# Kernel optimization log

Hardware: AMD Instinct MI355X
Metric: run time of the kernel (lower is better)

The kernel has to match this reference:

```python
import jax, jax.numpy as jnp
import numpy as np

H = 1024      # hidden_size
I = 2048      # intermediate_size
E = 32        # num_routed_experts
B, S = 4, 2048


def setup_inputs() -> dict:
    key = jax.random.key(0)
    ks = jax.random.split(key, 8)
    scale = 0.02
    inp = {
        "hidden_states": jax.random.normal(ks[0], (B, S, H), dtype=jnp.float32),
        # router gate: stored [H, E] so logits = x @ gate_w
        "gate_w": jax.random.normal(ks[1], (H, E), dtype=jnp.float32) * scale,
        # shared SwiGLU (num_shared_experts=1), weights stored [in, out]
        "shared_gate_w": jax.random.normal(ks[2], (H, I), dtype=jnp.float32) * scale,
        "shared_up_w": jax.random.normal(ks[3], (H, I), dtype=jnp.float32) * scale,
        "shared_down_w": jax.random.normal(ks[4], (I, H), dtype=jnp.float32) * scale,
        # routed grouped SwiGLU, weights stored [E, in, out] (matches GroupedLinear)
        "routed_gate_w": jax.random.normal(ks[5], (E, H, I), dtype=jnp.float32) * scale,
        "routed_up_w": jax.random.normal(ks[6], (E, H, I), dtype=jnp.float32) * scale,
        "routed_down_w": jax.random.normal(ks[7], (E, I, H), dtype=jnp.float32) * scale,
    }
    return inp


def _grouped_mm(a, w, group_sizes):
    # a: [T, in], w: [E, in, out], group_sizes: [E] int32 -> [T, out]
    return jax.lax.ragged_dot(a, w, group_sizes)


def _swiglu(x, gw, uw, dw):
    return (jax.nn.silu(x @ gw) * (x @ uw)) @ dw


def reference(hidden_states, gate_w, shared_gate_w, shared_up_w, shared_down_w,
              routed_gate_w, routed_up_w, routed_down_w):
    b, s, h = hidden_states.shape
    x = hidden_states.reshape(-1, h)                      # [T, H]

    # ---- shared expert ----
    shared_out = _swiglu(x, shared_gate_w, shared_up_w, shared_down_w)

    # ---- router: top-1 ----
    logits = x @ gate_w                                   # [T, E]
    topk_ids = jnp.argmax(logits, axis=-1)                # [T]
    topk_val = jnp.max(logits, axis=-1)                   # [T]
    scores = jax.nn.sigmoid(topk_val)[:, None]            # [T, 1]
    xs = x * scores                                       # scale tokens by router score

    # ---- dispatch: sort tokens by expert id ----
    tokens_per_expert = jnp.zeros((E,), jnp.int32).at[topk_ids].add(1)
    order = jnp.argsort(topk_ids)                         # token ids sorted by expert
    sorted_x = xs[order]                                  # [T, H]

    # ---- grouped SwiGLU experts ----
    g = _grouped_mm(sorted_x, routed_gate_w, tokens_per_expert)   # [T, I]
    u = _grouped_mm(sorted_x, routed_up_w, tokens_per_expert)     # [T, I]
    d = _grouped_mm(jax.nn.silu(g) * u, routed_down_w, tokens_per_expert)  # [T, H]

    # ---- combine: unsort back to token order ----
    inv = jnp.argsort(order)
    routed_out = d[inv]

    return (shared_out + routed_out).reshape(b, s, h)
```

## Files before the change

### kernel.cpp

```cpp
#include <hip/hip_runtime.h>
#include <stdint.h>
#include <stddef.h>

#define TOK 8192
#define H 1024
#define IDIM 2048
#define NE 32
#define BM 128
#define BN 64
#define BK 64
#define MAX_TILES 96

typedef __attribute__((ext_vector_type(8))) short short8;
typedef __attribute__((ext_vector_type(4))) float f32x4;
typedef __attribute__((ext_vector_type(4))) float float4v;
typedef __attribute__((ext_vector_type(2))) unsigned int uint2v;


__device__ __forceinline__ unsigned short f2bf(float x) {
  unsigned u = __builtin_bit_cast(unsigned, x);
  u += 0x7fffu + ((u >> 16) & 1u);
  return (unsigned short)(u >> 16);
}

__device__ __forceinline__ void gll16(const void* g, void* l) {
  __builtin_amdgcn_global_load_lds(
      (const __attribute__((address_space(1))) unsigned int*)g,
      (__attribute__((address_space(3))) unsigned int*)l, 16, 0, 0);
}

__device__ __forceinline__ f32x4 mfma16(short8 a, short8 b, f32x4 c) {
  return __builtin_amdgcn_mfma_f32_16x16x32_bf16(a, b, c, 0, 0, 0);
}

__device__ __forceinline__ int wswz(int n) {
  return ((n ^ (n >> 2)) & 7) << 4;
}


__global__ __launch_bounds__(256) void router_kernel(
    const float* __restrict__ x, const float* __restrict__ gw,
    unsigned short* __restrict__ xbf, unsigned short* __restrict__ xsbf,
    int* __restrict__ expert_id, int* __restrict__ counts)
{
  __shared__ float xl[8 * H];
  __shared__ float plog[8][8][NE];
  __shared__ float sscore[8];
  const int tid = threadIdx.x;
  const long t0 = (long)blockIdx.x * 8;

  const float4v* src = (const float4v*)(x + t0 * H);
  float4v* dst = (float4v*)xl;
  #pragma unroll
  for (int i = 0; i < 8; ++i) dst[tid + i * 256] = src[tid + i * 256];
  __syncthreads();

  {
    const int e = tid & 31, c = tid >> 5;
    float acc[8] = {0, 0, 0, 0, 0, 0, 0, 0};
    const float* gp = gw + (c * 128) * NE + e;
    for (int h = 0; h < 128; ++h) {
      float g = gp[h * NE];
      const float* xr = xl + (c * 128 + h);
      #pragma unroll
      for (int tk = 0; tk < 8; ++tk) acc[tk] += xr[tk * H] * g;
    }
    #pragma unroll
    for (int tk = 0; tk < 8; ++tk) plog[c][tk][e] = acc[tk];
  }
  __syncthreads();
  {
    const int e = tid & 31, tok = tid >> 5;
    float lg = 0.f;
    #pragma unroll
    for (int c = 0; c < 8; ++c) lg += plog[c][tok][e];
    float m = lg; int be = e;
    #pragma unroll
    for (int mask = 16; mask >= 1; mask >>= 1) {
      float om = __shfl_xor(m, mask);
      int   oe = __shfl_xor(be, mask);
      if (om > m || (om == m && oe < be)) { m = om; be = oe; }
    }
    if (e == 0) {
      sscore[tok] = 1.f / (1.f + __expf(-m));
      expert_id[t0 + tok] = be;
      atomicAdd(&counts[be], 1);
    }
  }
  __syncthreads();
  {
    const float sc = sscore[tid >> 5];
    const int base = (tid >> 5) * H + (tid & 31) * 32;
    #pragma unroll
    for (int i = 0; i < 4; ++i) {
      short8 vx, vs;
      #pragma unroll
      for (int j = 0; j < 8; ++j) {
        float v = xl[base + i * 8 + j];
        vx[j] = (short)f2bf(v);
        vs[j] = (short)f2bf(v * sc);
      }
      *(short8*)(xbf  + t0 * H + base + i * 8) = vx;
      *(short8*)(xsbf + t0 * H + base + i * 8) = vs;
    }
  }
}


__global__ void scan_kernel(const int* __restrict__ counts, int* __restrict__ offsets,
                            int* __restrict__ cursor, int* __restrict__ tile_e,
                            int* __restrict__ tile_p, int* __restrict__ n_tiles)
{
  if (threadIdx.x != 0) return;
  int off = 0, nt = 0;
  for (int e = 0; e < NE; ++e) {
    offsets[e] = off; cursor[e] = off;
    int cc = counts[e];
    for (int k = 0; k < cc; k += BM) { tile_e[nt] = e; tile_p[nt] = off + k; ++nt; }
    off += cc;
  }
  offsets[NE] = off;
  n_tiles[0] = nt;
}


__global__ __launch_bounds__(256) void perm_kernel(
    const int* __restrict__ expert_id, int* __restrict__ cursor, int* __restrict__ perm)
{
  int t = blockIdx.x * 256 + threadIdx.x;
  int e = expert_id[t];
  int pos = atomicAdd(&cursor[e], 1);
  perm[pos] = t;
}


template<bool ROUTED>
__global__ __launch_bounds__(256, 2) void gateup_kernel(
    const unsigned short* __restrict__ Abase,
    const float* __restrict__ WgAll, const float* __restrict__ WuAll,
    unsigned short* __restrict__ act,
    const int* __restrict__ perm, const int* __restrict__ tile_e,
    const int* __restrict__ tile_p, const int* __restrict__ offsets,
    const int* __restrict__ n_tiles)
{
  __shared__ short Alds[2][BM * BK];
  __shared__ short Glds[BN * BK];
  __shared__ short Ulds[BN * BK];

  const int tid = threadIdx.x;
  const int wave = tid >> 6, lane = tid & 63;

  int row0, row_end;
  const float *Wg, *Wu;
  if constexpr (ROUTED) {
    if ((int)blockIdx.x >= *n_tiles) return;
    const int e = tile_e[blockIdx.x];
    row0 = tile_p[blockIdx.x];
    row_end = offsets[e + 1];
    Wg = WgAll + (size_t)e * H * IDIM;
    Wu = WuAll + (size_t)e * H * IDIM;
  } else {
    row0 = blockIdx.x * BM; row_end = row0 + BM;
    Wg = WgAll; Wu = WuAll;
  }
  const int n0 = blockIdx.y * BN;

  const unsigned short* asrc[4];
  int aoff[4];
  #pragma unroll
  for (int i = 0; i < 4; ++i) {
    const int r = i * 32 + wave * 8 + (lane >> 3);
    int grow;
    if constexpr (ROUTED) {
      int p = row0 + r;
      if (p >= row_end) p = row0;
      grow = perm[p];
    } else grow = row0 + r;
    const int cb = ((lane & 7) * 16) ^ ((r & 7) << 4);
    asrc[i] = Abase + (size_t)grow * H + (cb >> 1);
    aoff[i] = (i * 32 + wave * 8) * BK;
  }

  const int wq = tid >> 4;
  const int wc = tid & 15;

  f32x4 accg[2][4] = {};
  f32x4 accu[2][4] = {};
  float4v g4[4], u4[4];

  auto stageA = [&](int k0, int buf) {
    #pragma unroll
    for (int i = 0; i < 4; ++i) gll16(asrc[i] + k0, &Alds[buf][aoff[i]]);
  };
  auto loadW = [&](int k0) {
    #pragma unroll
    for (int r = 0; r < 4; ++r) {
      const size_t goff = (size_t)(k0 + wq * 4 + r) * IDIM + (n0 + wc * 4);
      g4[r] = *(const float4v*)(Wg + goff);
      u4[r] = *(const float4v*)(Wu + goff);
    }
  };
  auto writeW = [&]() {
    #pragma unroll
    for (int j = 0; j < 4; ++j) {
      const int n = wc * 4 + j;
      const int cb = (wq * 8) ^ wswz(n);
      uint2v pg, pu;
      pg.x = (unsigned)f2bf(g4[0][j]) | ((unsigned)f2bf(g4[1][j]) << 16);
      pg.y = (unsigned)f2bf(g4[2][j]) | ((unsigned)f2bf(g4[3][j]) << 16);
      pu.x = (unsigned)f2bf(u4[0][j]) | ((unsigned)f2bf(u4[1][j]) << 16);
      pu.y = (unsigned)f2bf(u4[2][j]) | ((unsigned)f2bf(u4[3][j]) << 16);
      *(uint2v*)((char*)Glds + n * 128 + cb) = pg;
      *(uint2v*)((char*)Ulds + n * 128 + cb) = pu;
    }
  };
  auto compute = [&](int buf) {
    #pragma unroll
    for (int kk = 0; kk < 2; ++kk) {
      short8 af[2];
      #pragma unroll
      for (int m = 0; m < 2; ++m) {
        const int r = wave * 32 + m * 16 + (lane & 15);
        const int cb = (kk * 64 + ((lane >> 4) * 16)) ^ ((r & 7) << 4);
        af[m] = *(const short8*)((const char*)Alds[buf] + r * 128 + cb);
      }
      #pragma unroll
      for (int nf = 0; nf < 4; ++nf) {
        const int n = nf * 16 + (lane & 15);
        const int cb = (kk * 64 + ((lane >> 4) * 16)) ^ wswz(n);
        short8 bg = *(const short8*)((const char*)Glds + n * 128 + cb);
        short8 bu = *(const short8*)((const char*)Ulds + n * 128 + cb);
        #pragma unroll
        for (int m = 0; m < 2; ++m) {
          accg[m][nf] = mfma16(af[m], bg, accg[m][nf]);
          accu[m][nf] = mfma16(af[m], bu, accu[m][nf]);
        }
      }
    }
  };

  stageA(0, 0);
  loadW(0);
  writeW();
  __syncthreads();

  int cur = 0;
  #pragma unroll 1
  for (int kt = 0; kt < H / BK - 1; ++kt) {
    stageA((kt + 1) * BK, cur ^ 1);
    loadW((kt + 1) * BK);
    compute(cur);
    __syncthreads();
    writeW();
    __syncthreads();
    cur ^= 1;
  }
  compute(cur);

  #pragma unroll
  for (int m = 0; m < 2; ++m)
    #pragma unroll
    for (int nf = 0; nf < 4; ++nf) {
      const int col = n0 + nf * 16 + (lane & 15);
      #pragma unroll
      for (int j = 0; j < 4; ++j) {
        const int row = row0 + wave * 32 + m * 16 + ((lane >> 4) * 4) + j;
        if (ROUTED && row >= row_end) continue;
        const float g = accg[m][nf][j];
        const float u = accu[m][nf][j];
        const float v = (g / (1.f + __expf(-g))) * u;
        act[(size_t)row * IDIM + col] = f2bf(v);
      }
    }
}


template<bool ROUTED>
__global__ __launch_bounds__(256, 2) void down_kernel(
    const unsigned short* __restrict__ act,
    const float* __restrict__ WdAll,
    float* __restrict__ out,
    const int* __restrict__ perm, const int* __restrict__ tile_e,
    const int* __restrict__ tile_p, const int* __restrict__ offsets,
    const int* __restrict__ n_tiles)
{
  __shared__ short Alds[2][BM * BK];
  __shared__ short Wlds[BN * BK];

  const int tid = threadIdx.x;
  const int wave = tid >> 6, lane = tid & 63;

  int row0, row_end;
  const float* Wd;
  if constexpr (ROUTED) {
    if ((int)blockIdx.x >= *n_tiles) return;
    const int e = tile_e[blockIdx.x];
    row0 = tile_p[blockIdx.x];
    row_end = offsets[e + 1];
    Wd = WdAll + (size_t)e * IDIM * H;
  } else {
    row0 = blockIdx.x * BM; row_end = row0 + BM;
    Wd = WdAll;
  }
  const int n0 = blockIdx.y * BN;

  const unsigned short* asrc[4];
  int aoff[4];
  #pragma unroll
  for (int i = 0; i < 4; ++i) {
    const int r = i * 32 + wave * 8 + (lane >> 3);
    int p = row0 + r;
    if (ROUTED && p >= row_end) p = row0;
    const int cb = ((lane & 7) * 16) ^ ((r & 7) << 4);
    asrc[i] = act + (size_t)p * IDIM + (cb >> 1);
    aoff[i] = (i * 32 + wave * 8) * BK;
  }

  const int wq = tid >> 4;
  const int wc = tid & 15;

  f32x4 acc[2][4] = {};
  float4v w4[4];

  auto stageA = [&](int k0, int buf) {
    #pragma unroll
    for (int i = 0; i < 4; ++i) gll16(asrc[i] + k0, &Alds[buf][aoff[i]]);
  };
  auto loadW = [&](int k0) {
    #pragma unroll
    for (int r = 0; r < 4; ++r)
      w4[r] = *(const float4v*)(Wd + (size_t)(k0 + wq * 4 + r) * H + (n0 + wc * 4));
  };
  auto writeW = [&]() {
    #pragma unroll
    for (int j = 0; j < 4; ++j) {
      const int n = wc * 4 + j;
      const int cb = (wq * 8) ^ wswz(n);
      uint2v pw;
      pw.x = (unsigned)f2bf(w4[0][j]) | ((unsigned)f2bf(w4[1][j]) << 16);
      pw.y = (unsigned)f2bf(w4[2][j]) | ((unsigned)f2bf(w4[3][j]) << 16);
      *(uint2v*)((char*)Wlds + n * 128 + cb) = pw;
    }
  };
  auto compute = [&](int buf) {
    #pragma unroll
    for (int kk = 0; kk < 2; ++kk) {
      short8 af[2];
      #pragma unroll
      for (int m = 0; m < 2; ++m) {
        const int r = wave * 32 + m * 16 + (lane & 15);
        const int cb = (kk * 64 + ((lane >> 4) * 16)) ^ ((r & 7) << 4);
        af[m] = *(const short8*)((const char*)Alds[buf] + r * 128 + cb);
      }
      #pragma unroll
      for (int nf = 0; nf < 4; ++nf) {
        const int n = nf * 16 + (lane & 15);
        const int cb = (kk * 64 + ((lane >> 4) * 16)) ^ wswz(n);
        short8 bw = *(const short8*)((const char*)Wlds + n * 128 + cb);
        #pragma unroll
        for (int m = 0; m < 2; ++m) acc[m][nf] = mfma16(af[m], bw, acc[m][nf]);
      }
    }
  };

  stageA(0, 0);
  loadW(0);
  writeW();
  __syncthreads();

  int cur = 0;
  #pragma unroll 1
  for (int kt = 0; kt < IDIM / BK - 1; ++kt) {
    stageA((kt + 1) * BK, cur ^ 1);
    loadW((kt + 1) * BK);
    compute(cur);
    __syncthreads();
    writeW();
    __syncthreads();
    cur ^= 1;
  }
  compute(cur);

  #pragma unroll
  for (int m = 0; m < 2; ++m)
    #pragma unroll
    for (int nf = 0; nf < 4; ++nf) {
      const int col = n0 + nf * 16 + (lane & 15);
      #pragma unroll
      for (int j = 0; j < 4; ++j) {
        const int row = row0 + wave * 32 + m * 16 + ((lane >> 4) * 4) + j;
        const float v = acc[m][nf][j];
        if constexpr (ROUTED) {
          if (row < row_end) {
            const int t = perm[row];
            out[(size_t)t * H + col] += v;
          }
        } else {
          out[(size_t)row * H + col] = v;
        }
      }
    }
}


extern "C" void kernel_launch(void* const* d_in, const int* in_sizes, int n_in,
                              void* d_out, int out_size, void* d_ws, size_t ws_size,
                              hipStream_t stream) {
  (void)in_sizes; (void)n_in; (void)out_size; (void)ws_size;
  const float* x      = (const float*)d_in[0];
  const float* gate_w = (const float*)d_in[1];
  const float* sgw    = (const float*)d_in[2];
  const float* suw    = (const float*)d_in[3];
  const float* sdw    = (const float*)d_in[4];
  const float* rgw    = (const float*)d_in[5];
  const float* ruw    = (const float*)d_in[6];
  const float* rdw    = (const float*)d_in[7];
  float* out = (float*)d_out;

  char* ws = (char*)d_ws;
  unsigned short* xbf  = (unsigned short*)(ws + 0);
  unsigned short* xsbf = (unsigned short*)(ws + 16777216);
  unsigned short* act  = (unsigned short*)(ws + 33554432);
  int* perm      = (int*)(ws + 67108864);
  int* expert_id = (int*)(ws + 67141632);
  int* counts    = (int*)(ws + 67174400);
  int* offsets   = (int*)(ws + 67174528);
  int* cursor    = (int*)(ws + 67174784);
  int* tile_e    = (int*)(ws + 67174912);
  int* tile_p    = (int*)(ws + 67175424);
  int* n_tiles   = (int*)(ws + 67175936);

  hipMemsetAsync(counts, 0, NE * sizeof(int), stream);
  router_kernel<<<TOK / 8, 256, 0, stream>>>(x, gate_w, xbf, xsbf, expert_id, counts);
  scan_kernel<<<1, 64, 0, stream>>>(counts, offsets, cursor, tile_e, tile_p, n_tiles);
  perm_kernel<<<TOK / 256, 256, 0, stream>>>(expert_id, cursor, perm);

  gateup_kernel<false><<<dim3(TOK / BM, IDIM / BN), 256, 0, stream>>>(
      xbf, sgw, suw, act, perm, tile_e, tile_p, offsets, n_tiles);
  down_kernel<false><<<dim3(TOK / BM, H / BN), 256, 0, stream>>>(
      act, sdw, out, perm, tile_e, tile_p, offsets, n_tiles);
  gateup_kernel<true><<<dim3(MAX_TILES, IDIM / BN), 256, 0, stream>>>(
      xsbf, rgw, ruw, act, perm, tile_e, tile_p, offsets, n_tiles);
  down_kernel<true><<<dim3(MAX_TILES, H / BN), 256, 0, stream>>>(
      act, rdw, out, perm, tile_e, tile_p, offsets, n_tiles);
}
```

Baseline: 714.9 us.

## Widen GEMM N tile to 128 with a 2x2 wave layout per block

Doubles the output tile width from 64 to 128 columns and arranges the four waves in a 2x2 grid, each computing a 64x64 sub-tile (4x4 MFMA fragments). Each thread now loads 8 weight rows and writes 16-byte packed bf16 vectors into LDS. The aim is to reuse each staged A tile across twice as many columns, which halves the number of A reloads and blocks. In exchange, accumulator registers double (32 f32x4 for gate/up), which may push VGPR pressure against the launch bound of 2 blocks per CU, and the larger weight LDS tiles reduce occupancy headroom.

```diff
diff --git a/kernel.cpp b/kernel.cpp
--- a/kernel.cpp
+++ b/kernel.cpp
@@ -7,14 +7,14 @@
 #define IDIM 2048
 #define NE 32
 #define BM 128
-#define BN 64
+#define BN 128
 #define BK 64
 #define MAX_TILES 96
 
 typedef __attribute__((ext_vector_type(8))) short short8;
 typedef __attribute__((ext_vector_type(4))) float f32x4;
 typedef __attribute__((ext_vector_type(4))) float float4v;
-typedef __attribute__((ext_vector_type(2))) unsigned int uint2v;
+typedef __attribute__((ext_vector_type(4))) unsigned int uint4v;
 
 
 __device__ __forceinline__ unsigned short f2bf(float x) {
@@ -149,6 +149,7 @@
 
   const int tid = threadIdx.x;
   const int wave = tid >> 6, lane = tid & 63;
+  const int wm = wave >> 1, wn = wave & 1;
 
   int row0, row_end;
   const float *Wg, *Wu;
@@ -169,7 +170,7 @@
   int aoff[4];
   #pragma unroll
   for (int i = 0; i < 4; ++i) {
-    const int r = i * 32 + wave * 8 + (lane >> 3);
+    const int r = wave * 32 + i * 8 + (lane >> 3);
     int grow;
     if constexpr (ROUTED) {
       int p = row0 + r;
@@ -178,24 +179,26 @@
     } else grow = row0 + r;
     const int cb = ((lane & 7) * 16) ^ ((r & 7) << 4);
     asrc[i] = Abase + (size_t)grow * H + (cb >> 1);
-    aoff[i] = (i * 32 + wave * 8) * BK;
-  }
-
-  const int wq = tid >> 4;
-  const int wc = tid & 15;
-
-  f32x4 accg[2][4] = {};
-  f32x4 accu[2][4] = {};
-  float4v g4[4], u4[4];
-
-  auto stageA = [&](int k0, int buf) {
-    #pragma unroll
-    for (int i = 0; i < 4; ++i) gll16(asrc[i] + k0, &Alds[buf][aoff[i]]);
-  };
-  auto loadW = [&](int k0) {
-    #pragma unroll
-    for (int r = 0; r < 4; ++r) {
-      const size_t goff = (size_t)(k0 + wq * 4 + r) * IDIM + (n0 + wc * 4);
+    aoff[i] = (wave * 32 + i * 8) * BK;
+  }
+
+  const int wq = tid >> 5;
+  const int wc = tid & 31;
+
+  f32x4 accg[4][4] = {};
+  f32x4 accu[4][4] = {};
+  float4v g4[8], u4[8];
+
+  auto stageA = [&](int kt) {
+    short* base = Alds[kt & 1];
+    #pragma unroll
+    for (int i = 0; i < 4; ++i) gll16(asrc[i] + kt * BK, base + aoff[i]);
+  };
+  auto loadW = [&](int kt) {
+    const int k0 = kt * BK;
+    #pragma unroll
+    for (int r = 0; r < 8; ++r) {
+      const size_t goff = (size_t)(k0 + wq * 8 + r) * IDIM + (n0 + wc * 4);
       g4[r] = *(const float4v*)(Wg + goff);
       u4[r] = *(const float4v*)(Wu + goff);
     }
@@ -204,34 +207,39 @@
     #pragma unroll
     for (int j = 0; j < 4; ++j) {
       const int n = wc * 4 + j;
-      const int cb = (wq * 8) ^ wswz(n);
-      uint2v pg, pu;
+      const int cb = (wq * 16) ^ wswz(n);
+      uint4v pg, pu;
       pg.x = (unsigned)f2bf(g4[0][j]) | ((unsigned)f2bf(g4[1][j]) << 16);
       pg.y = (unsigned)f2bf(g4[2][j]) | ((unsigned)f2bf(g4[3][j]) << 16);
+      pg.z = (unsigned)f2bf(g4[4][j]) | ((unsigned)f2bf(g4[5][j]) << 16);
+      pg.w = (unsigned)f2bf(g4[6][j]) | ((unsigned)f2bf(g4[7][j]) << 16);
       pu.x = (unsigned)f2bf(u4[0][j]) | ((unsigned)f2bf(u4[1][j]) << 16);
       pu.y = (unsigned)f2bf(u4[2][j]) | ((unsigned)f2bf(u4[3][j]) << 16);
-      *(uint2v*)((char*)Glds + n * 128 + cb) = pg;
-      *(uint2v*)((char*)Ulds + n * 128 + cb) = pu;
-    }
-  };
-  auto compute = [&](int buf) {
+      pu.z = (unsigned)f2bf(u4[4][j]) | ((unsigned)f2bf(u4[5][j]) << 16);
+      pu.w = (unsigned)f2bf(u4[6][j]) | ((unsigned)f2bf(u4[7][j]) << 16);
+      *(uint4v*)((char*)Glds + n * 128 + cb) = pg;
+      *(uint4v*)((char*)Ulds + n * 128 + cb) = pu;
+    }
+  };
+  auto compute = [&](int kt) {
+    const char* ab = (const char*)Alds[kt & 1];
     #pragma unroll
     for (int kk = 0; kk < 2; ++kk) {
-      short8 af[2];
-      #pragma unroll
-      for (int m = 0; m < 2; ++m) {
-        const int r = wave * 32 + m * 16 + (lane & 15);
+      short8 af[4];
+      #pragma unroll
+      for (int m = 0; m < 4; ++m) {
+        const int r = wm * 64 + m * 16 + (lane & 15);
         const int cb = (kk * 64 + ((lane >> 4) * 16)) ^ ((r & 7) << 4);
-        af[m] = *(const short8*)((const char*)Alds[buf] + r * 128 + cb);
+        af[m] = *(const short8*)(ab + r * 128 + cb);
       }
       #pragma unroll
       for (int nf = 0; nf < 4; ++nf) {
-        const int n = nf * 16 + (lane & 15);
+        const int n = wn * 64 + nf * 16 + (lane & 15);
         const int cb = (kk * 64 + ((lane >> 4) * 16)) ^ wswz(n);
         short8 bg = *(const short8*)((const char*)Glds + n * 128 + cb);
         short8 bu = *(const short8*)((const char*)Ulds + n * 128 + cb);
         #pragma unroll
-        for (int m = 0; m < 2; ++m) {
+        for (int m = 0; m < 4; ++m) {
           accg[m][nf] = mfma16(af[m], bg, accg[m][nf]);
           accu[m][nf] = mfma16(af[m], bu, accu[m][nf]);
         }
@@ -239,32 +247,30 @@
     }
   };
 
-  stageA(0, 0);
+  stageA(0);
   loadW(0);
   writeW();
   __syncthreads();
 
-  int cur = 0;
   #pragma unroll 1
   for (int kt = 0; kt < H / BK - 1; ++kt) {
-    stageA((kt + 1) * BK, cur ^ 1);
-    loadW((kt + 1) * BK);
-    compute(cur);
+    stageA(kt + 1);
+    loadW(kt + 1);
+    compute(kt);
     __syncthreads();
     writeW();
     __syncthreads();
-    cur ^= 1;
-  }
-  compute(cur);
+  }
+  compute(H / BK - 1);
 
   #pragma unroll
-  for (int m = 0; m < 2; ++m)
+  for (int m = 0; m < 4; ++m)
     #pragma unroll
     for (int nf = 0; nf < 4; ++nf) {
-      const int col = n0 + nf * 16 + (lane & 15);
+      const int col = n0 + wn * 64 + nf * 16 + (lane & 15);
       #pragma unroll
       for (int j = 0; j < 4; ++j) {
-        const int row = row0 + wave * 32 + m * 16 + ((lane >> 4) * 4) + j;
+        const int row = row0 + wm * 64 + m * 16 + ((lane >> 4) * 4) + j;
         if (ROUTED && row >= row_end) continue;
         const float g = accg[m][nf][j];
         const float u = accu[m][nf][j];
@@ -289,6 +295,7 @@
 
   const int tid = threadIdx.x;
   const int wave = tid >> 6, lane = tid & 63;
+  const int wm = wave >> 1, wn = wave & 1;
 
   int row0, row_end;
   const float* Wd;
@@ -308,87 +315,90 @@
   int aoff[4];
   #pragma unroll
   for (int i = 0; i < 4; ++i) {
-    const int r = i * 32 + wave * 8 + (lane >> 3);
+    const int r = wave * 32 + i * 8 + (lane >> 3);
     int p = row0 + r;
     if (ROUTED && p >= row_end) p = row0;
     const int cb = ((lane & 7) * 16) ^ ((r & 7) << 4);
     asrc[i] = act + (size_t)p * IDIM + (cb >> 1);
-    aoff[i] = (i * 32 + wave * 8) * BK;
-  }
-
-  const int wq = tid >> 4;
-  const int wc = tid & 15;
-
-  f32x4 acc[2][4] = {};
-  float4v w4[4];
-
-  auto stageA = [&](int k0, int buf) {
-    #pragma unroll
-    for (int i = 0; i < 4; ++i) gll16(asrc[i] + k0, &Alds[buf][aoff[i]]);
-  };
-  auto loadW = [&](int k0) {
-    #pragma unroll
-    for (int r = 0; r < 4; ++r)
-      w4[r] = *(const float4v*)(Wd + (size_t)(k0 + wq * 4 + r) * H + (n0 + wc * 4));
+    aoff[i] = (wave * 32 + i * 8) * BK;
+  }
+
+  const int wq = tid >> 5;
+  const int wc = tid & 31;
+
+  f32x4 acc[4][4] = {};
+  float4v w4[8];
+
+  auto stageA = [&](int kt) {
+    short* base = Alds[kt & 1];
+    #pragma unroll
+    for (int i = 0; i < 4; ++i) gll16(asrc[i] + kt * BK, base + aoff[i]);
+  };
+  auto loadW = [&](int kt) {
+    const int k0 = kt * BK;
+    #pragma unroll
+    for (int r = 0; r < 8; ++r)
+      w4[r] = *(const float4v*)(Wd + (size_t)(k0 + wq * 8 + r) * H + (n0 + wc * 4));
   };
   auto writeW = [&]() {
     #pragma unroll
     for (int j = 0; j < 4; ++j) {
       const int n = wc * 4 + j;
-      const int cb = (wq * 8) ^ wswz(n);
-      uint2v pw;
+      const int cb = (wq * 16) ^ wswz(n);
+      uint4v pw;
       pw.x = (unsigned)f2bf(w4[0][j]) | ((unsigned)f2bf(w4[1][j]) << 16);
       pw.y = (unsigned)f2bf(w4[2][j]) | ((unsigned)f2bf(w4[3][j]) << 16);
-      *(uint2v*)((char*)Wlds + n * 128 + cb) = pw;
-    }
-  };
-  auto compute = [&](int buf) {
+      pw.z = (unsigned)f2bf(w4[4][j]) | ((unsigned)f2bf(w4[5][j]) << 16);
+      pw.w = (unsigned)f2bf(w4[6][j]) | ((unsigned)f2bf(w4[7][j]) << 16);
+      *(uint4v*)((char*)Wlds + n * 128 + cb) = pw;
+    }
+  };
+  auto compute = [&](int kt) {
+    const char* ab = (const char*)Alds[kt & 1];
     #pragma unroll
     for (int kk = 0; kk < 2; ++kk) {
-      short8 af[2];
-      #pragma unroll
-      for (int m = 0; m < 2; ++m) {
-        const int r = wave * 32 + m * 16 + (lane & 15);
+      short8 af[4];
+      #pragma unroll
+      for (int m = 0; m < 4; ++m) {
+        const int r = wm * 64 + m * 16 + (lane & 15);
         const int cb = (kk * 64 + ((lane >> 4) * 16)) ^ ((r & 7) << 4);
-        af[m] = *(const short8*)((const char*)Alds[buf] + r * 128 + cb);
+        af[m] = *(const short8*)(ab + r * 128 + cb);
       }
       #pragma unroll
       for (int nf = 0; nf < 4; ++nf) {
-        const int n = nf * 16 + (lane & 15);
+        const int n = wn * 64 + nf * 16 + (lane & 15);
         const int cb = (kk * 64 + ((lane >> 4) * 16)) ^ wswz(n);
         short8 bw = *(const short8*)((const char*)Wlds + n * 128 + cb);
         #pragma unroll
-        for (int m = 0; m < 2; ++m) acc[m][nf] = mfma16(af[m], bw, acc[m][nf]);
-      }
-    }
-  };
-
-  stageA(0, 0);
+        for (int m = 0; m < 4; ++m) acc[m][nf] = mfma16(af[m], bw, acc[m][nf]);
+      }
+    }
+  };
+
+  stageA(0);
   loadW(0);
   writeW();
   __syncthreads();
 
-  int cur = 0;
   #pragma unroll 1
   for (int kt = 0; kt < IDIM / BK - 1; ++kt) {
-    stageA((kt + 1) * BK, cur ^ 1);
-    loadW((kt + 1) * BK);
-    compute(cur);
+    stageA(kt + 1);
+    loadW(kt + 1);
+    compute(kt);
     __syncthreads();
     writeW();
     __syncthreads();
-    cur ^= 1;
-  }
-  compute(cur);
+  }
+  compute(IDIM / BK - 1);
 
   #pragma unroll
-  for (int m = 0; m < 2; ++m)
+  for (int m = 0; m < 4; ++m)
     #pragma unroll
     for (int nf = 0; nf < 4; ++nf) {
-      const int col = n0 + nf * 16 + (lane & 15);
+      const int col = n0 + wn * 64 + nf * 16 + (lane & 15);
       #pragma unroll
       for (int j = 0; j < 4; ++j) {
-        const int row = row0 + wave * 32 + m * 16 + ((lane >> 4) * 4) + j;
+        const int row = row0 + wm * 64 + m * 16 + ((lane >> 4) * 4) + j;
         const float v = acc[m][nf][j];
         if constexpr (ROUTED) {
           if (row < row_end) {
```

Result: faster. 671.9 us (-6.0%).
